# Performance work log

Hardware: AMD Instinct MI355X
Metric: run time of the kernel (lower is better)

The kernel has to match this reference:

```python
import jax, jax.numpy as jnp
import numpy as np

B, S, D, H = 4, 2048, 1024, 16
HD = D // H
THETA = 10000.0


def rope(x, pos, theta=THETA):
    # x: [..., seq, d], pos: broadcastable to [..., seq]
    d = x.shape[-1]
    half = d // 2
    inv_freq = 1.0 / (theta ** (jnp.arange(half, dtype=jnp.float32) * 2.0 / d))  # [half]
    ang = pos[..., None].astype(jnp.float32) * inv_freq  # [..., seq, half]
    cos, sin = jnp.cos(ang), jnp.sin(ang)
    x1, x2 = x[..., 0::2], x[..., 1::2]
    r1 = x1 * cos - x2 * sin
    r2 = x1 * sin + x2 * cos
    return jnp.stack([r1, r2], axis=-1).reshape(x.shape).astype(x.dtype)


def setup_inputs() -> dict:
    key = jax.random.key(0)
    ks = jax.random.split(key, 5)
    x = jax.random.normal(ks[0], (B, S, D), dtype=jnp.float32)
    token_positions = jnp.tile(jnp.arange(S, dtype=jnp.int64 if jax.config.jax_enable_x64 else jnp.int32), (B, 1))
    scale = 0.02
    Wq = jax.random.normal(ks[1], (D, D), dtype=jnp.float32) * scale
    Wk = jax.random.normal(ks[2], (D, D), dtype=jnp.float32) * scale
    Wv = jax.random.normal(ks[3], (D, D), dtype=jnp.float32) * scale
    Wo = jax.random.normal(ks[4], (D, D), dtype=jnp.float32) * scale
    return {"x": x, "token_positions": token_positions, "Wq": Wq, "Wk": Wk, "Wv": Wv, "Wo": Wo}


def reference(x, token_positions, Wq, Wk, Wv, Wo):
    b, s, d = x.shape
    # QKV projections (torch Linear: x @ W.T), split heads -> [b, h, s, hd]
    def proj(W):
        y = jnp.einsum('bsd,ed->bse', x, W)
        return y.reshape(b, s, H, HD).transpose(0, 2, 1, 3)
    Q, K, V = proj(Wq), proj(Wk), proj(Wv)
    # token_positions [..., seq] -> [..., 1, seq] to broadcast over heads
    pos = token_positions[:, None, :]  # [b, 1, s]
    Q = rope(Q, pos)
    K = rope(K, pos)
    # causal mask and scaled dot-product attention
    idx = jnp.arange(s)
    causal = idx[:, None] >= idx[None, :]  # [s, s], query >= key
    scores = jnp.einsum('bhqd,bhkd->bhqk', Q, K) / jnp.sqrt(jnp.float32(HD))
    scores = jnp.where(causal, scores, -jnp.inf)
    weights = jax.nn.softmax(scores, axis=-1)
    o = jnp.einsum('bhqk,bhkd->bhqd', weights, V)
    o = o.transpose(0, 2, 1, 3).reshape(b, s, d)  # merge heads
    return jnp.einsum('bsd,ed->bse', o, Wo)
```

## Files before the change

kernel.cpp:

```cpp
#include <hip/hip_runtime.h>

#define S_LEN 2048
#define NH 16
#define HDIM 64
#define DMODEL 1024

typedef __attribute__((ext_vector_type(8))) short bf16x8;
typedef __attribute__((ext_vector_type(4))) float f32x4;

__device__ __forceinline__ short f2bf(float f) {
    union { float f; unsigned u; } x; x.f = f;
    unsigned r = x.u + 0x7fffu + ((x.u >> 16) & 1u);
    return (short)(r >> 16);
}

#define GLDS(g, l) __builtin_amdgcn_global_load_lds( \
    (__attribute__((address_space(1))) void*)(g),    \
    (__attribute__((address_space(3))) void*)(l), 16, 0, 0)

#define QSCALE 0.18033688011112042f
#define FREQ_L 0.41524101186109327f

__global__ __launch_bounds__(256) void prep(const float* __restrict__ x,
                                            const float* __restrict__ wq,
                                            const float* __restrict__ wk,
                                            const float* __restrict__ wv,
                                            const float* __restrict__ wo,
                                            const int* __restrict__ tp,
                                            short* __restrict__ xb,
                                            short* __restrict__ wqb,
                                            short* __restrict__ wkb,
                                            short* __restrict__ wvb,
                                            short* __restrict__ wob,
                                            float2* __restrict__ tab) {
    int bid = blockIdx.x;
    if (bid < 8192) {
        int i = bid * 256 + threadIdx.x;
        float4 v = ((const float4*)x)[i];
        short4 o;
        o.x = f2bf(v.x); o.y = f2bf(v.y); o.z = f2bf(v.z); o.w = f2bf(v.w);
        ((short4*)xb)[i] = o;
    } else if (bid < 12288) {
        int sel = (bid - 8192) >> 10;
        const float* in = sel == 0 ? wq : sel == 1 ? wk : sel == 2 ? wv : wo;
        short* out = sel == 0 ? wqb : sel == 1 ? wkb : sel == 2 ? wvb : wob;
        int i = ((bid - 8192) & 1023) * 256 + threadIdx.x;
        float4 v = ((const float4*)in)[i];
        short4 o;
        o.x = f2bf(v.x); o.y = f2bf(v.y); o.z = f2bf(v.z); o.w = f2bf(v.w);
        ((short4*)out)[i] = o;
    } else {
        int idx = (bid - 12288) * 256 + threadIdx.x;
        int b = idx >> 16, s = (idx >> 5) & 2047, i = idx & 31;
        float p = (float)tp[(b << 11) + s];
        float freq = exp2f(-(float)i * FREQ_L);
        float sn, cs;
        sincosf(p * freq, &sn, &cs);
        tab[idx] = make_float2(cs, sn);
    }
}

__global__ __launch_bounds__(256) void gemm_qkv(const short* __restrict__ A,
                                                const short* __restrict__ Bq,
                                                const short* __restrict__ Bk,
                                                const short* __restrict__ Bv,
                                                const float2* __restrict__ tab,
                                                short* __restrict__ Qo,
                                                short* __restrict__ Ko,
                                                short* __restrict__ Vo) {
    constexpr int K = 1024, BK = 32;
    __shared__ __align__(16) short sa[3][128 * BK];
    __shared__ __align__(16) short sb[3][128 * BK];

    const int sel = blockIdx.x >> 3;
    const int bn = blockIdx.x & 7;
    const int bm = blockIdx.y;
    const short* Bm = sel == 0 ? Bq : sel == 1 ? Bk : Bv;
    short* Cb = sel == 0 ? Qo : sel == 1 ? Ko : Vo;

    const int tid = threadIdx.x;
    const int lane = tid & 63;
    const int w = tid >> 6;
    const int wm = w >> 1, wn = w & 1;
    const int quad = lane >> 4, l16 = lane & 15;

    int aoff[2], boff[2];
#pragma unroll
    for (int i = 0; i < 2; i++) {
        int cs = i * 256 + tid;
        int row = cs >> 2;
        int gc = (cs & 3) ^ ((row >> 1) & 3);
        aoff[i] = (bm * 128 + row) * K + gc * 8;
        boff[i] = (bn * 128 + row) * K + gc * 8;
    }

    auto stage = [&](int kt, int b) {
        const int k0 = kt * BK;
#pragma unroll
        for (int i = 0; i < 2; i++)
            GLDS(A + aoff[i] + k0, (char*)&sa[b][0] + i * 4096 + w * 1024);
#pragma unroll
        for (int i = 0; i < 2; i++)
            GLDS(Bm + boff[i] + k0, (char*)&sb[b][0] + i * 4096 + w * 1024);
    };

    f32x4 acc[4][4] = {};
    const int rsw = (quad ^ ((l16 >> 1) & 3)) * 8;

    auto compute = [&](int b) {
        bf16x8 af[4];
#pragma unroll
        for (int mi = 0; mi < 4; mi++)
            af[mi] = *(const bf16x8*)&sa[b][(wm * 64 + mi * 16 + l16) * BK + rsw];
#pragma unroll
        for (int ni = 0; ni < 4; ni++) {
            bf16x8 bfr = *(const bf16x8*)&sb[b][(wn * 64 + ni * 16 + l16) * BK + rsw];
#pragma unroll
            for (int mi = 0; mi < 4; mi++)
                acc[mi][ni] = __builtin_amdgcn_mfma_f32_16x16x32_bf16(af[mi], bfr,
                                                                     acc[mi][ni], 0, 0, 0);
        }
    };

    stage(0, 0);
    stage(1, 1);

    auto step = [&](int kt, int b, int bs) {
        asm volatile("s_waitcnt vmcnt(4)" ::: "memory");
        __builtin_amdgcn_s_barrier();
        __builtin_amdgcn_sched_barrier(0);
        stage(kt + 2, bs);
        compute(b);
    };

    for (int kt = 0; kt < 30; kt += 3) {
        step(kt + 0, 0, 2);
        step(kt + 1, 1, 0);
        step(kt + 2, 2, 1);
    }
    asm volatile("s_waitcnt vmcnt(4)" ::: "memory");
    __builtin_amdgcn_s_barrier();
    __builtin_amdgcn_sched_barrier(0);
    compute(0);
    asm volatile("s_waitcnt vmcnt(0)" ::: "memory");
    __builtin_amdgcn_s_barrier();
    __builtin_amdgcn_sched_barrier(0);
    compute(1);

    const int gm0 = bm * 128 + wm * 64;
    const int gn0 = bn * 128 + wn * 64;

    if (sel == 2) {
#pragma unroll
        for (int mi = 0; mi < 4; mi++)
#pragma unroll
            for (int ni = 0; ni < 4; ni++)
#pragma unroll
                for (int r = 0; r < 4; r++) {
                    int gm = gm0 + mi * 16 + quad * 4 + r;
                    int gn = gn0 + ni * 16 + l16;
                    int b = gm >> 11, s = gm & 2047;
                    int h = gn >> 6,  hd = gn & 63;
                    Cb[((b * NH + h) * HDIM + hd) * S_LEN + s] = f2bf(acc[mi][ni][r]);
                }
    } else {
        const float qs = (sel == 0) ? QSCALE : 1.0f;
#pragma unroll
        for (int mi = 0; mi < 4; mi++)
#pragma unroll
            for (int r = 0; r < 4; r++) {
                int gm = gm0 + mi * 16 + quad * 4 + r;
                const float2* trow = tab + (gm << 5);
                int b = gm >> 11, s = gm & 2047;
#pragma unroll
                for (int ni = 0; ni < 4; ni++) {
                    float2 cs = trow[ni * 8 + (l16 >> 1)];
                    float v = acc[mi][ni][r];
                    float prt = __shfl_xor(v, 1, 64);
                    float val = (l16 & 1) ? (prt * cs.y + v * cs.x)
                                          : (v * cs.x - prt * cs.y);
                    int gn = gn0 + ni * 16 + l16;
                    int h = gn >> 6, hd = gn & 63;
                    Cb[((b * NH + h) * S_LEN + s) * HDIM + hd] = f2bf(val * qs);
                }
            }
    }
}

__global__ __launch_bounds__(256) void gemm_o(const short* __restrict__ A,
                                              const short* __restrict__ Bw,
                                              float* __restrict__ Cf) {
    constexpr int N = 1024, K = 1024, BK = 32;
    __shared__ __align__(16) short sa[3][128 * BK];
    __shared__ __align__(16) short sb[3][64 * BK];

    const int tid = threadIdx.x;
    const int lane = tid & 63;
    const int w = tid >> 6;
    const int quad = lane >> 4, l16 = lane & 15;
    const int bn = blockIdx.x, bm = blockIdx.y;
    const int arow0 = bm * 128, brow0 = bn * 64;

    int aoff[2], boff;
#pragma unroll
    for (int i = 0; i < 2; i++) {
        int cs = i * 256 + tid;
        int row = cs >> 2;
        int gc = (cs & 3) ^ ((row >> 1) & 3);
        aoff[i] = (arow0 + row) * K + gc * 8;
    }
    {
        int row = tid >> 2;
        int gc = (tid & 3) ^ ((row >> 1) & 3);
        boff = (brow0 + row) * K + gc * 8;
    }

    auto stage = [&](int kt, int b) {
        const int k0 = kt * BK;
#pragma unroll
        for (int i = 0; i < 2; i++)
            GLDS(A + aoff[i] + k0, (char*)&sa[b][0] + i * 4096 + w * 1024);
        GLDS(Bw + boff + k0, (char*)&sb[b][0] + w * 1024);
    };

    f32x4 acc[2][4] = {};
    const int rsw = (quad ^ ((l16 >> 1) & 3)) * 8;

    auto compute = [&](int b) {
        bf16x8 af[2];
#pragma unroll
        for (int mi = 0; mi < 2; mi++)
            af[mi] = *(const bf16x8*)&sa[b][(w * 32 + mi * 16 + l16) * BK + rsw];
#pragma unroll
        for (int ni = 0; ni < 4; ni++) {
            bf16x8 bfr = *(const bf16x8*)&sb[b][(ni * 16 + l16) * BK + rsw];
#pragma unroll
            for (int mi = 0; mi < 2; mi++)
                acc[mi][ni] = __builtin_amdgcn_mfma_f32_16x16x32_bf16(af[mi], bfr,
                                                                     acc[mi][ni], 0, 0, 0);
        }
    };

    stage(0, 0);
    stage(1, 1);

    auto step = [&](int kt, int b, int bs) {
        asm volatile("s_waitcnt vmcnt(3)" ::: "memory");
        __builtin_amdgcn_s_barrier();
        __builtin_amdgcn_sched_barrier(0);
        stage(kt + 2, bs);
        compute(b);
    };

    for (int kt = 0; kt < 30; kt += 3) {
        step(kt + 0, 0, 2);
        step(kt + 1, 1, 0);
        step(kt + 2, 2, 1);
    }
    asm volatile("s_waitcnt vmcnt(3)" ::: "memory");
    __builtin_amdgcn_s_barrier();
    __builtin_amdgcn_sched_barrier(0);
    compute(0);
    asm volatile("s_waitcnt vmcnt(0)" ::: "memory");
    __builtin_amdgcn_s_barrier();
    __builtin_amdgcn_sched_barrier(0);
    compute(1);

    const int gm0 = arow0 + w * 32;
#pragma unroll
    for (int mi = 0; mi < 2; mi++)
#pragma unroll
        for (int ni = 0; ni < 4; ni++)
#pragma unroll
            for (int r = 0; r < 4; r++) {
                int gm = gm0 + mi * 16 + quad * 4 + r;
                int gn = brow0 + ni * 16 + l16;
                Cf[gm * N + gn] = acc[mi][ni][r];
            }
}

__global__ __launch_bounds__(256, 3) void attn(const short* __restrict__ Q,
                                               const short* __restrict__ Km,
                                               const short* __restrict__ Vt,
                                               short* __restrict__ O) {
    __shared__ __align__(16) short kbuf[2][64 * 64];
    __shared__ __align__(16) short vbuf[2][64 * 64];
    __shared__ __align__(16) short pbuf[4][32 * 64];

    const int lane = threadIdx.x & 63;
    const int w = threadIdx.x >> 6;
    const int quad = lane >> 4, l16 = lane & 15;
    const int l7 = l16 & 7;
    const int bh = blockIdx.y;

    const short* Qg = Q  + bh * S_LEN * 64;
    const short* Kg = Km + bh * S_LEN * 64;
    const short* Vg = Vt + bh * 64 * S_LEN;
    short* myp = &pbuf[w][0];

    const int b = bh >> 4, h = bh & 15;

    bf16x8 ones;
#pragma unroll
    for (int j = 0; j < 8; j++) ones[j] = (short)0x3f80;

    auto stage = [&](int kt, int par) {
        const short* kt_base = Kg + kt * 64 * 64;
        const short* vt_base = Vg + kt * 64;
#pragma unroll
        for (int i = 0; i < 2; ++i) {
            int ch = w * 128 + i * 64 + lane;
            int row = ch >> 3;
            int c = (ch & 7) ^ (row & 7);
            GLDS(kt_base + row * 64 + c * 8, (char*)&kbuf[par][(w * 128 + i * 64) * 8]);
        }
#pragma unroll
        for (int i = 0; i < 2; ++i) {
            int ch = w * 128 + i * 64 + lane;
            int row = ch >> 3;
            int c = (ch & 7) ^ (row & 7);
            GLDS(vt_base + row * S_LEN + c * 8, (char*)&vbuf[par][(w * 128 + i * 64) * 8]);
        }
    };

    const int QtA = blockIdx.x;
    const int QtB = 15 - blockIdx.x;

    stage(0, 0);
    int t = 0;

    for (int phase = 0; phase < 2; ++phase) {
        const int Qt = phase ? QtB : QtA;
        const int nkt = 2 * Qt + 2;

        bf16x8 aq[2][2];
#pragma unroll
        for (int mi = 0; mi < 2; mi++) {
            int qrow = Qt * 128 + w * 32 + mi * 16 + l16;
#pragma unroll
            for (int kc = 0; kc < 2; kc++)
                aq[mi][kc] = *(const bf16x8*)&Qg[qrow * 64 + kc * 32 + quad * 8];
        }

        f32x4 oacc[2][4] = {};
        f32x4 lacc[2] = {};

        for (int kt = 0; kt < nkt; ++kt, ++t) {
            __syncthreads();
            if (kt + 1 < nkt)    stage(kt + 1, (t + 1) & 1);
            else if (phase == 0) stage(0,      (t + 1) & 1);
            const short* kb_cur = &kbuf[t & 1][0];
            const short* vb_cur = &vbuf[t & 1][0];

            f32x4 sc[2][4] = {};
#pragma unroll
            for (int nt = 0; nt < 4; nt++) {
                int raddr = (nt * 16 + l16) * 64;
#pragma unroll
                for (int kc = 0; kc < 2; kc++) {
                    bf16x8 kf = *(const bf16x8*)&kb_cur[raddr + (((quad + kc * 4) ^ l7) * 8)];
                    sc[0][nt] = __builtin_amdgcn_mfma_f32_16x16x32_bf16(aq[0][kc], kf, sc[0][nt], 0, 0, 0);
                    sc[1][nt] = __builtin_amdgcn_mfma_f32_16x16x32_bf16(aq[1][kc], kf, sc[1][nt], 0, 0, 0);
                }
            }
            if (kt >= nkt - 2) {
#pragma unroll
                for (int mi = 0; mi < 2; mi++)
#pragma unroll
                    for (int nt = 0; nt < 4; nt++)
#pragma unroll
                        for (int r = 0; r < 4; r++) {
                            int col = kt * 64 + nt * 16 + l16;
                            int row = Qt * 128 + w * 32 + mi * 16 + quad * 4 + r;
                            if (col > row) sc[mi][nt][r] = -__builtin_inff();
                        }
            }
#pragma unroll
            for (int mi = 0; mi < 2; mi++)
#pragma unroll
                for (int nt = 0; nt < 4; nt++)
#pragma unroll
                    for (int r = 0; r < 4; r++) {
                        float pv = __builtin_amdgcn_exp2f(sc[mi][nt][r]);
                        int q = mi * 16 + quad * 4 + r;
                        union { float f; unsigned short us[2]; } uu;
                        uu.f = pv;
                        myp[q * 64 + (((nt * 2 + (l16 >> 3)) ^ (q & 7)) * 8) + l7] =
                            (short)uu.us[1];
                    }
            bf16x8 ap[2][2];
#pragma unroll
            for (int mi = 0; mi < 2; mi++)
#pragma unroll
                for (int kc = 0; kc < 2; kc++)
                    ap[mi][kc] = *(const bf16x8*)&myp[(mi * 16 + l16) * 64 +
                                                      (((quad + kc * 4) ^ l7) * 8)];
#pragma unroll
            for (int nt = 0; nt < 4; nt++) {
                int raddr = (nt * 16 + l16) * 64;
#pragma unroll
                for (int kc = 0; kc < 2; kc++) {
                    bf16x8 vf = *(const bf16x8*)&vb_cur[raddr + (((quad + kc * 4) ^ l7) * 8)];
                    oacc[0][nt] = __builtin_amdgcn_mfma_f32_16x16x32_bf16(ap[0][kc], vf, oacc[0][nt], 0, 0, 0);
                    oacc[1][nt] = __builtin_amdgcn_mfma_f32_16x16x32_bf16(ap[1][kc], vf, oacc[1][nt], 0, 0, 0);
                }
            }
#pragma unroll
            for (int mi = 0; mi < 2; mi++) {
                lacc[mi] = __builtin_amdgcn_mfma_f32_16x16x32_bf16(ap[mi][0], ones, lacc[mi], 0, 0, 0);
                lacc[mi] = __builtin_amdgcn_mfma_f32_16x16x32_bf16(ap[mi][1], ones, lacc[mi], 0, 0, 0);
            }
        }
#pragma unroll
        for (int mi = 0; mi < 2; mi++)
#pragma unroll
            for (int r = 0; r < 4; r++) {
                float inv = 1.0f / lacc[mi][r];
                int srow = Qt * 128 + w * 32 + mi * 16 + quad * 4 + r;
#pragma unroll
                for (int nt = 0; nt < 4; nt++) {
                    int hd = nt * 16 + l16;
                    O[(b * S_LEN + srow) * DMODEL + h * HDIM + hd] = f2bf(oacc[mi][nt][r] * inv);
                }
            }
    }
}

extern "C" void kernel_launch(void* const* d_in, const int* in_sizes, int n_in,
                              void* d_out, int out_size, void* d_ws, size_t ws_size,
                              hipStream_t stream) {
    const float* x  = (const float*)d_in[0];
    const int*   tp = (const int*)d_in[1];
    const float* Wq = (const float*)d_in[2];
    const float* Wk = (const float*)d_in[3];
    const float* Wv = (const float*)d_in[4];
    const float* Wo = (const float*)d_in[5];
    float* out = (float*)d_out;

    char* ws = (char*)d_ws;
    const size_t MB = 1024 * 1024;
    short* xb  = (short*)(ws);
    short* wqb = (short*)(ws + 16 * MB);
    short* wkb = (short*)(ws + 18 * MB);
    short* wvb = (short*)(ws + 20 * MB);
    short* wob = (short*)(ws + 22 * MB);
    short* Qb  = (short*)(ws + 24 * MB);
    short* Kb  = (short*)(ws + 40 * MB);
    short* Vtb = (short*)(ws + 56 * MB);
    float2* tab = (float2*)d_out;

    prep<<<13312, 256, 0, stream>>>(x, Wq, Wk, Wv, Wo, tp,
                                    xb, wqb, wkb, wvb, wob, tab);

    gemm_qkv<<<dim3(24, 64), 256, 0, stream>>>(xb, wqb, wkb, wvb, tab, Qb, Kb, Vtb);

    attn<<<dim3(8, 64), 256, 0, stream>>>(Qb, Kb, Vtb, xb);

    gemm_o<<<dim3(16, 64), 256, 0, stream>>>(xb, wob, out);
}
```

Baseline: 276.0 us.

## Use BK=64 single-buffer QKV GEMM and stage transposed V output through LDS

```diff
diff --git a/kernel.cpp b/kernel.cpp
--- a/kernel.cpp
+++ b/kernel.cpp
@@ -68,9 +68,10 @@
                                                 short* __restrict__ Qo,
                                                 short* __restrict__ Ko,
                                                 short* __restrict__ Vo) {
-    constexpr int K = 1024, BK = 32;
-    __shared__ __align__(16) short sa[3][128 * BK];
-    __shared__ __align__(16) short sb[3][128 * BK];
+    constexpr int K = 1024, BK = 64;
+    __shared__ __align__(16) short smem[2 * 128 * BK];
+    short* sa = smem;
+    short* sb = smem + 128 * BK;
 
     const int sel = blockIdx.x >> 3;
     const int bn = blockIdx.x & 7;
@@ -83,86 +84,81 @@
     const int w = tid >> 6;
     const int wm = w >> 1, wn = w & 1;
     const int quad = lane >> 4, l16 = lane & 15;
-
-    int aoff[2], boff[2];
-#pragma unroll
-    for (int i = 0; i < 2; i++) {
-        int cs = i * 256 + tid;
-        int row = cs >> 2;
-        int gc = (cs & 3) ^ ((row >> 1) & 3);
-        aoff[i] = (bm * 128 + row) * K + gc * 8;
-        boff[i] = (bn * 128 + row) * K + gc * 8;
-    }
-
-    auto stage = [&](int kt, int b) {
-        const int k0 = kt * BK;
-#pragma unroll
-        for (int i = 0; i < 2; i++)
-            GLDS(A + aoff[i] + k0, (char*)&sa[b][0] + i * 4096 + w * 1024);
-#pragma unroll
-        for (int i = 0; i < 2; i++)
-            GLDS(Bm + boff[i] + k0, (char*)&sb[b][0] + i * 4096 + w * 1024);
-    };
+    const int l7 = l16 & 7;
+
+    int aoff[4], boff[4];
+#pragma unroll
+    for (int i = 0; i < 4; i++) {
+        int Lc = i * 256 + tid;
+        int row = Lc >> 3;
+        int cc = (Lc & 7) ^ (row & 7);
+        aoff[i] = (bm * 128 + row) * K + cc * 8;
+        boff[i] = (bn * 128 + row) * K + cc * 8;
+    }
 
     f32x4 acc[4][4] = {};
-    const int rsw = (quad ^ ((l16 >> 1) & 3)) * 8;
-
-    auto compute = [&](int b) {
-        bf16x8 af[4];
-#pragma unroll
-        for (int mi = 0; mi < 4; mi++)
-            af[mi] = *(const bf16x8*)&sa[b][(wm * 64 + mi * 16 + l16) * BK + rsw];
-#pragma unroll
-        for (int ni = 0; ni < 4; ni++) {
-            bf16x8 bfr = *(const bf16x8*)&sb[b][(wn * 64 + ni * 16 + l16) * BK + rsw];
+
+    for (int k0 = 0; k0 < K; k0 += BK) {
+#pragma unroll
+        for (int i = 0; i < 4; i++)
+            GLDS(A + aoff[i] + k0, (char*)sa + i * 4096 + w * 1024);
+#pragma unroll
+        for (int i = 0; i < 4; i++)
+            GLDS(Bm + boff[i] + k0, (char*)sb + i * 4096 + w * 1024);
+        __syncthreads();
+
+#pragma unroll
+        for (int kc = 0; kc < 2; kc++) {
+            const int c = ((kc * 4 + quad) ^ l7) * 8;
+            bf16x8 af[4], bfm[4];
 #pragma unroll
             for (int mi = 0; mi < 4; mi++)
-                acc[mi][ni] = __builtin_amdgcn_mfma_f32_16x16x32_bf16(af[mi], bfr,
-                                                                     acc[mi][ni], 0, 0, 0);
-        }
-    };
-
-    stage(0, 0);
-    stage(1, 1);
-
-    auto step = [&](int kt, int b, int bs) {
-        asm volatile("s_waitcnt vmcnt(4)" ::: "memory");
-        __builtin_amdgcn_s_barrier();
-        __builtin_amdgcn_sched_barrier(0);
-        stage(kt + 2, bs);
-        compute(b);
-    };
-
-    for (int kt = 0; kt < 30; kt += 3) {
-        step(kt + 0, 0, 2);
-        step(kt + 1, 1, 0);
-        step(kt + 2, 2, 1);
-    }
-    asm volatile("s_waitcnt vmcnt(4)" ::: "memory");
-    __builtin_amdgcn_s_barrier();
-    __builtin_amdgcn_sched_barrier(0);
-    compute(0);
-    asm volatile("s_waitcnt vmcnt(0)" ::: "memory");
-    __builtin_amdgcn_s_barrier();
-    __builtin_amdgcn_sched_barrier(0);
-    compute(1);
+                af[mi] = *(const bf16x8*)&sa[(wm * 64 + mi * 16 + l16) * BK + c];
+#pragma unroll
+            for (int ni = 0; ni < 4; ni++)
+                bfm[ni] = *(const bf16x8*)&sb[(wn * 64 + ni * 16 + l16) * BK + c];
+#pragma unroll
+            for (int mi = 0; mi < 4; mi++)
+#pragma unroll
+                for (int ni = 0; ni < 4; ni++)
+                    acc[mi][ni] = __builtin_amdgcn_mfma_f32_16x16x32_bf16(af[mi], bfm[ni],
+                                                                          acc[mi][ni], 0, 0, 0);
+        }
+        __syncthreads();
+    }
 
     const int gm0 = bm * 128 + wm * 64;
     const int gn0 = bn * 128 + wn * 64;
 
     if (sel == 2) {
-#pragma unroll
-        for (int mi = 0; mi < 4; mi++)
-#pragma unroll
-            for (int ni = 0; ni < 4; ni++)
-#pragma unroll
-                for (int r = 0; r < 4; r++) {
-                    int gm = gm0 + mi * 16 + quad * 4 + r;
-                    int gn = gn0 + ni * 16 + l16;
-                    int b = gm >> 11, s = gm & 2047;
-                    int h = gn >> 6,  hd = gn & 63;
-                    Cb[((b * NH + h) * HDIM + hd) * S_LEN + s] = f2bf(acc[mi][ni][r]);
-                }
+        short* T = smem;
+#pragma unroll
+        for (int mi = 0; mi < 4; mi++) {
+            int lmb = wm * 64 + mi * 16 + quad * 4;
+#pragma unroll
+            for (int ni = 0; ni < 4; ni++) {
+                int ln = wn * 64 + ni * 16 + l16;
+                short4 pk;
+                pk.x = f2bf(acc[mi][ni][0]);
+                pk.y = f2bf(acc[mi][ni][1]);
+                pk.z = f2bf(acc[mi][ni][2]);
+                pk.w = f2bf(acc[mi][ni][3]);
+                *(short4*)&T[ln * 128 + (lmb ^ ((ln & 15) << 3))] = pk;
+            }
+        }
+        __syncthreads();
+        const int row = tid >> 1, half = tid & 1;
+        const int grow = bn * 128 + row;
+        const int gb = (bm * 128) >> 11;
+        const int gs0 = (bm * 128) & 2047;
+        short* dst = Cb + (((size_t)(gb * NH + (grow >> 6)) * HDIM + (grow & 63)) * S_LEN
+                           + gs0 + half * 64);
+#pragma unroll
+        for (int j = 0; j < 8; j++) {
+            bf16x8 v = *(const bf16x8*)&T[row * 128 +
+                        ((half * 64 + j * 8) ^ ((row & 15) << 3))];
+            *(bf16x8*)(dst + j * 8) = v;
+        }
     } else {
         const float qs = (sel == 0) ? QSCALE : 1.0f;
 #pragma unroll
```

After: 263.6 us. 1.05x faster.
